# Optimization experiments

Hardware: AMD Instinct MI355X
Metric: run time of the kernel (lower is better)

Reference implementation:

```python
import jax, jax.numpy as jnp
import numpy as np

T, B, E, H, V = 256, 256, 256, 512, 50257
FORGET_BIAS = 1.0  # tf BasicLSTMCell default


def setup_inputs() -> dict:
    key = jax.random.key(0)
    k1, k2, k3, k4 = jax.random.split(key, 4)
    x = jax.random.normal(k1, (T, B, E), dtype=jnp.float32)
    # BasicLSTMCell kernel: [(E+H), 4H], gate order i, j, f, o
    lstm_kernel = jax.random.normal(k2, (E + H, 4 * H), dtype=jnp.float32) * 0.05
    lstm_bias = jnp.zeros((4 * H,), dtype=jnp.float32)
    W_out = jax.random.normal(k3, (H, V), dtype=jnp.float32) * 0.05
    b_out = jax.random.normal(k4, (V,), dtype=jnp.float32) * 0.05
    return {"x": x, "lstm_kernel": lstm_kernel, "lstm_bias": lstm_bias,
            "W_out": W_out, "b_out": b_out}


def reference(x, lstm_kernel, lstm_bias, W_out, b_out):
    # x: [T, B, E] (static_rnn list of timesteps). BasicLSTMCell recurrence.
    h0 = jnp.zeros((x.shape[1], H), dtype=x.dtype)
    c0 = jnp.zeros_like(h0)

    def step(carry, x_t):
        h, c = carry
        gates = jnp.concatenate([x_t, h], axis=-1) @ lstm_kernel + lstm_bias
        i, j, f, o = jnp.split(gates, 4, axis=-1)  # tf gate order: i, j, f, o
        c_new = jax.nn.sigmoid(f + FORGET_BIAS) * c + jax.nn.sigmoid(i) * jnp.tanh(j)
        h_new = jax.nn.sigmoid(o) * jnp.tanh(c_new)
        return (h_new, c_new), None

    (h_last, _), _ = jax.lax.scan(step, (h0, c0), x)
    # Final dense projection on last output only
    return h_last @ W_out + b_out  # [B, V]
```

## Files before the change

### kernel.cpp

```cpp
#include <hip/hip_runtime.h>
#include <hip/hip_bf16.h>

#define T_DIM 256
#define B_DIM 256
#define E_DIM 256
#define H_DIM 512
#define V_DIM 50257
#define BH    (B_DIM * H_DIM)
#define PRE_AHEAD 5
#define SENT  0x7F7F7F7Fu

typedef __attribute__((ext_vector_type(8))) short short8;
typedef __attribute__((ext_vector_type(4))) float f32x4;
typedef __attribute__((ext_vector_type(4))) unsigned int uint4v;
typedef __attribute__((ext_vector_type(2))) unsigned int uint2v;

__device__ __forceinline__ unsigned short f2bf(float f) {
    union { float f; unsigned u; } v; v.f = f;
    unsigned r = v.u + 0x7FFFu + ((v.u >> 16) & 1u);
    return (unsigned short)(r >> 16);
}
__device__ __forceinline__ short cvt_bf(float f) { return (short)f2bf(f); }
__device__ __forceinline__ float sigmoidf_(float x) {
    return 1.0f / (1.0f + __expf(-x));
}
__device__ __forceinline__ float tanhf_(float x) {
    float xc = fminf(fmaxf(x, -15.0f), 15.0f);
    float e = __expf(2.0f * xc);
    return (e - 1.0f) / (e + 1.0f);
}

__device__ __forceinline__ short8 load16_mall(const unsigned short* p) {
    short8 r;
    asm volatile("global_load_dwordx4 %0, %1, off sc0 sc1"
                 : "=v"(r) : "v"(p) : "memory");
    return r;
}
__device__ __forceinline__ void store8_mall(unsigned short* p, uint2v v) {
    asm volatile("global_store_dwordx2 %0, %1, off sc0 sc1"
                 :: "v"(p), "v"(v) : "memory");
}
__device__ __forceinline__ bool frag_ready(short8 v) {
    union { short8 s; uint4v u; } c; c.s = v;
    return (c.u[0] != SENT) & (c.u[1] != SENT) & (c.u[2] != SENT) & (c.u[3] != SENT);
}

__global__ void __launch_bounds__(128, 1)
lstm_persist(const float* __restrict__ x,
             const float* __restrict__ wk,
             const float* __restrict__ bias,
             unsigned short* __restrict__ hbuf)
{
    extern __shared__ unsigned short lds_w[];
    const int tid = threadIdx.x;
    const int blk = blockIdx.x;
    const int bg  = blk & 7;
    const int hg  = blk >> 3;
    const int bb  = bg * 32;
    const int hh  = hg * 16;

    for (int f = 0; f < 96; ++f) {
        const int kt = f >> 2, g = f & 3;
        for (int idx = tid; idx < 512; idx += 128) {
            const int c  = idx & 15;
            const int hi = (idx >> 4) & 3;
            const int j  = idx >> 6;
            const int k  = kt * 32 + hi * 8 + j;
            const int col = g * 512 + hh + c;
            lds_w[(f * 64 + hi * 16 + c) * 8 + j] = f2bf(wk[(size_t)k * 2048 + col]);
        }
    }
    __syncthreads();

    const int w    = tid >> 6;
    const int lane = tid & 63;
    const int lc   = lane & 15;
    const int lk   = lane >> 4;

    const f32x4 bi  = *(const f32x4*)(bias + 0 * 512 + hh + lk * 4);
    const f32x4 bj  = *(const f32x4*)(bias + 1 * 512 + hh + lk * 4);
    f32x4       bf_ = *(const f32x4*)(bias + 2 * 512 + hh + lk * 4);
    const f32x4 bo  = *(const f32x4*)(bias + 3 * 512 + hh + lk * 4);
    bf_ = bf_ + 1.0f;

    f32x4 c_frag = {0.f, 0.f, 0.f, 0.f};

    const int arow = bb + w * 16 + lc;
    const float* xbase = x + (size_t)arow * E_DIM + lk * 8;
    const size_t hrow_off = (size_t)arow * H_DIM + lk * 8;
    const size_t hsto_off = (size_t)arow * H_DIM + hh + lk * 4;

    f32x4 xreg[16];
    #pragma unroll
    for (int kt = 0; kt < 8; ++kt) {
        const float* p = xbase + kt * 32;
        xreg[2 * kt]     = *(const f32x4*)p;
        xreg[2 * kt + 1] = *(const f32x4*)(p + 4);
    }

    const uint2v sentv = {SENT, SENT};

    for (int t = 0; t < T_DIM; ++t) {
        f32x4 a0 = {0.f,0.f,0.f,0.f}, a1 = a0, a2 = a0, a3 = a0;
        short8 apk[8];
        #pragma unroll
        for (int kt = 0; kt < 8; ++kt) {
            const f32x4 lo = xreg[2 * kt];
            const f32x4 hi = xreg[2 * kt + 1];
            short8 a;
            a[0]=cvt_bf(lo[0]); a[1]=cvt_bf(lo[1]); a[2]=cvt_bf(lo[2]); a[3]=cvt_bf(lo[3]);
            a[4]=cvt_bf(hi[0]); a[5]=cvt_bf(hi[1]); a[6]=cvt_bf(hi[2]); a[7]=cvt_bf(hi[3]);
            apk[kt] = a;
        }
        #pragma unroll
        for (int kt = 0; kt < 8; ++kt) {
            const unsigned short* wp = lds_w + ((size_t)(kt * 4) * 64 + lane) * 8;
            a0 = __builtin_amdgcn_mfma_f32_16x16x32_bf16(*(const short8*)(wp +    0), apk[kt], a0, 0,0,0);
            a1 = __builtin_amdgcn_mfma_f32_16x16x32_bf16(*(const short8*)(wp +  512), apk[kt], a1, 0,0,0);
            a2 = __builtin_amdgcn_mfma_f32_16x16x32_bf16(*(const short8*)(wp + 1024), apk[kt], a2, 0,0,0);
            a3 = __builtin_amdgcn_mfma_f32_16x16x32_bf16(*(const short8*)(wp + 1536), apk[kt], a3, 0,0,0);
        }

        if (t + 1 < T_DIM) {
            const float* xn = xbase + (size_t)(t + 1) * (B_DIM * E_DIM);
            #pragma unroll
            for (int kt = 0; kt < 8; ++kt) {
                const float* p = xn + kt * 32;
                xreg[2 * kt]     = *(const f32x4*)p;
                xreg[2 * kt + 1] = *(const f32x4*)(p + 4);
            }
        }

        if (t > 0) {
            const unsigned short* hr = hbuf + (size_t)t * BH + hrow_off;
            short8 hfr[16];
            #pragma unroll
            for (int k = 0; k < 16; ++k)
                hfr[k] = load16_mall(hr + k * 32);
            asm volatile("s_waitcnt vmcnt(0)" ::: "memory");
            __builtin_amdgcn_sched_barrier(0);

            unsigned pend = 0;
            #pragma unroll
            for (int k = 0; k < 16; ++k)
                pend |= frag_ready(hfr[k]) ? 0u : (1u << k);
            #pragma unroll 1
            while (!__all(pend == 0)) {
                #pragma unroll
                for (int k = 0; k < 16; ++k)
                    if (pend & (1u << k)) hfr[k] = load16_mall(hr + k * 32);
                asm volatile("s_waitcnt vmcnt(0)" ::: "memory");
                __builtin_amdgcn_sched_barrier(0);
                unsigned np = 0;
                #pragma unroll
                for (int k = 0; k < 16; ++k)
                    if (pend & (1u << k))
                        np |= frag_ready(hfr[k]) ? 0u : (1u << k);
                pend = np;
            }
            __builtin_amdgcn_sched_barrier(0);

            #pragma unroll
            for (int k = 0; k < 16; ++k) {
                const unsigned short* wp = lds_w + ((size_t)((8 + k) * 4) * 64 + lane) * 8;
                a0 = __builtin_amdgcn_mfma_f32_16x16x32_bf16(*(const short8*)(wp +    0), hfr[k], a0, 0,0,0);
                a1 = __builtin_amdgcn_mfma_f32_16x16x32_bf16(*(const short8*)(wp +  512), hfr[k], a1, 0,0,0);
                a2 = __builtin_amdgcn_mfma_f32_16x16x32_bf16(*(const short8*)(wp + 1024), hfr[k], a2, 0,0,0);
                a3 = __builtin_amdgcn_mfma_f32_16x16x32_bf16(*(const short8*)(wp + 1536), hfr[k], a3, 0,0,0);
            }
        }

        unsigned short hu[4];
        #pragma unroll
        for (int j = 0; j < 4; ++j) {
            const float iv = a0[j] + bi[j];
            const float jv = a1[j] + bj[j];
            const float fv = a2[j] + bf_[j];
            const float ov = a3[j] + bo[j];
            const float cn = sigmoidf_(fv) * c_frag[j] + sigmoidf_(iv) * tanhf_(jv);
            c_frag[j] = cn;
            hu[j] = f2bf(sigmoidf_(ov) * tanhf_(cn));
        }
        uint2v pk;
        pk[0] = (unsigned)hu[0] | ((unsigned)hu[1] << 16);
        pk[1] = (unsigned)hu[2] | ((unsigned)hu[3] << 16);
        store8_mall(hbuf + (size_t)(t + 1) * BH + hsto_off, pk);
        if (t + PRE_AHEAD <= T_DIM)
            store8_mall(hbuf + (size_t)(t + PRE_AHEAD) * BH + hsto_off, sentv);
    }
}

__global__ void __launch_bounds__(256)
proj_gemm(const unsigned short* __restrict__ h,
          const float* __restrict__ wout,
          const float* __restrict__ bout,
          float* __restrict__ out)
{
    const int tid  = threadIdx.x;
    const int w    = tid >> 6;
    const int lane = tid & 63;
    const int lc   = lane & 15;
    const int lk   = lane >> 4;
    const int n0   = blockIdx.x * 128 + w * 32;

    f32x4 acc[16][2];
    #pragma unroll
    for (int mt = 0; mt < 16; ++mt) {
        acc[mt][0] = (f32x4){0.f,0.f,0.f,0.f};
        acc[mt][1] = (f32x4){0.f,0.f,0.f,0.f};
    }
    int ncl[2];
    ncl[0] = min(n0 + lc,      V_DIM - 1);
    ncl[1] = min(n0 + 16 + lc, V_DIM - 1);

    #pragma unroll 4
    for (int kt = 0; kt < 16; ++kt) {
        short8 bfr[2];
        #pragma unroll
        for (int nt = 0; nt < 2; ++nt) {
            #pragma unroll
            for (int j = 0; j < 8; ++j) {
                const int k = kt * 32 + lk * 8 + j;
                bfr[nt][j] = (short)f2bf(wout[(size_t)k * V_DIM + ncl[nt]]);
            }
        }
        #pragma unroll
        for (int mt = 0; mt < 16; ++mt) {
            const short8 a = *(const short8*)(h + (size_t)(mt * 16 + lc) * H_DIM
                                                + kt * 32 + lk * 8);
            acc[mt][0] = __builtin_amdgcn_mfma_f32_16x16x32_bf16(a, bfr[0], acc[mt][0], 0,0,0);
            acc[mt][1] = __builtin_amdgcn_mfma_f32_16x16x32_bf16(a, bfr[1], acc[mt][1], 0,0,0);
        }
    }

    #pragma unroll
    for (int nt = 0; nt < 2; ++nt) {
        const int n = n0 + nt * 16 + lc;
        if (n < V_DIM) {
            const float bb = bout[n];
            #pragma unroll
            for (int mt = 0; mt < 16; ++mt)
                #pragma unroll
                for (int j = 0; j < 4; ++j)
                    out[(size_t)(mt * 16 + lk * 4 + j) * V_DIM + n] = acc[mt][nt][j] + bb;
        }
    }
}

extern "C" void kernel_launch(void* const* d_in, const int* in_sizes, int n_in,
                              void* d_out, int out_size, void* d_ws, size_t ws_size,
                              hipStream_t stream) {
    const float* x    = (const float*)d_in[0];
    const float* wk   = (const float*)d_in[1];
    const float* bias = (const float*)d_in[2];
    const float* wout = (const float*)d_in[3];
    const float* bout = (const float*)d_in[4];
    float* out = (float*)d_out;

    unsigned short* hbuf = (unsigned short*)d_ws;

    hipMemsetAsync(hbuf, 0x7F, (size_t)PRE_AHEAD * BH * 2, stream);

    hipFuncSetAttribute((const void*)lstm_persist,
                        hipFuncAttributeMaxDynamicSharedMemorySize, 96 * 1024);

    hipLaunchKernelGGL(lstm_persist, dim3(256), dim3(128), 96 * 1024, stream,
                       x, wk, bias, hbuf);
    hipLaunchKernelGGL(proj_gemm, dim3((V_DIM + 127) / 128), dim3(256), 0, stream,
                       hbuf + (size_t)T_DIM * BH, wout, bout, out);
}
```

Measured before the change: 1.557 ms.

## Issue h loads early and overlap with x-part MFMAs via double-buffered x registers

Restructures the persistent LSTM step so the next-timestep x prefetch and the h-state fragment loads are issued before the x-contribution MFMAs. The spin-wait on sentinels then runs only after those MFMAs, hiding global/MALL latency behind compute. The x prefetch registers are double-buffered (xA/xB, loop unrolled by two) so the prefetch no longer overwrites the registers in use. This raises register pressure, and the x-part MFMAs now sit in the dependency window of the h loads.

```diff
diff --git a/kernel.cpp b/kernel.cpp
--- a/kernel.cpp
+++ b/kernel.cpp
@@ -15,6 +15,8 @@
 typedef __attribute__((ext_vector_type(4))) unsigned int uint4v;
 typedef __attribute__((ext_vector_type(2))) unsigned int uint2v;
 
+#define MFMA __builtin_amdgcn_mfma_f32_16x16x32_bf16
+
 __device__ __forceinline__ unsigned short f2bf(float f) {
     union { float f; unsigned u; } v; v.f = f;
     unsigned r = v.u + 0x7FFFu + ((v.u >> 16) & 1u);
@@ -43,6 +45,105 @@
 __device__ __forceinline__ bool frag_ready(short8 v) {
     union { short8 s; uint4v u; } c; c.s = v;
     return (c.u[0] != SENT) & (c.u[1] != SENT) & (c.u[2] != SENT) & (c.u[3] != SENT);
+}
+
+__device__ __forceinline__ void lstm_step(
+    int t, f32x4 (&xc)[16], f32x4 (&xn)[16],
+    const float* __restrict__ xrow,
+    unsigned short* __restrict__ hbuf,
+    size_t hrow_off, size_t hsto_off,
+    const unsigned short* __restrict__ lds_w, int lane,
+    const f32x4& bi, const f32x4& bj, const f32x4& bf_, const f32x4& bo,
+    f32x4& c_frag)
+{
+    {
+        const int tn = (t + 1 < T_DIM) ? t + 1 : t;
+        const float* xp = xrow + (size_t)tn * (B_DIM * E_DIM);
+        #pragma unroll
+        for (int k = 0; k < 8; ++k) {
+            xn[2 * k]     = *(const f32x4*)(xp + k * 32);
+            xn[2 * k + 1] = *(const f32x4*)(xp + k * 32 + 4);
+        }
+    }
+
+    const unsigned short* hr = hbuf + (size_t)t * BH + hrow_off;
+    short8 hfr[16];
+    if (t > 0) {
+        #pragma unroll
+        for (int k = 0; k < 16; ++k)
+            hfr[k] = load16_mall(hr + k * 32);
+    }
+
+    f32x4 a0 = {0.f,0.f,0.f,0.f}, a1 = a0, a2 = a0, a3 = a0;
+    #pragma unroll
+    for (int kt = 0; kt < 8; ++kt) {
+        const f32x4 lo = xc[2 * kt];
+        const f32x4 hi = xc[2 * kt + 1];
+        short8 a;
+        a[0]=cvt_bf(lo[0]); a[1]=cvt_bf(lo[1]); a[2]=cvt_bf(lo[2]); a[3]=cvt_bf(lo[3]);
+        a[4]=cvt_bf(hi[0]); a[5]=cvt_bf(hi[1]); a[6]=cvt_bf(hi[2]); a[7]=cvt_bf(hi[3]);
+        const unsigned short* wp = lds_w + ((size_t)(kt * 4) * 64 + lane) * 8;
+        a0 = MFMA(*(const short8*)(wp +    0), a, a0, 0,0,0);
+        a1 = MFMA(*(const short8*)(wp +  512), a, a1, 0,0,0);
+        a2 = MFMA(*(const short8*)(wp + 1024), a, a2, 0,0,0);
+        a3 = MFMA(*(const short8*)(wp + 1536), a, a3, 0,0,0);
+    }
+
+    if (t > 0) {
+        asm volatile("s_waitcnt vmcnt(0)" ::: "memory");
+        __builtin_amdgcn_sched_barrier(0);
+        unsigned pend = 0;
+        #pragma unroll
+        for (int k = 0; k < 16; ++k)
+            pend |= frag_ready(hfr[k]) ? 0u : (1u << k);
+        #pragma unroll 1
+        while (!__all(pend == 0)) {
+            #pragma unroll
+            for (int k = 0; k < 16; ++k)
+                if (pend & (1u << k)) hfr[k] = load16_mall(hr + k * 32);
+            asm volatile("s_waitcnt vmcnt(0)" ::: "memory");
+            __builtin_amdgcn_sched_barrier(0);
+            unsigned np = 0;
+            #pragma unroll
+            for (int k = 0; k < 16; ++k)
+                if (pend & (1u << k))
+                    np |= frag_ready(hfr[k]) ? 0u : (1u << k);
+            pend = np;
+        }
+        __builtin_amdgcn_sched_barrier(0);
+
+        #pragma unroll
+        for (int k = 0; k < 16; ++k) {
+            const unsigned short* wp = lds_w + ((size_t)((8 + k) * 4) * 64 + lane) * 8;
+            a0 = MFMA(*(const short8*)(wp +    0), hfr[k], a0, 0,0,0);
+            a1 = MFMA(*(const short8*)(wp +  512), hfr[k], a1, 0,0,0);
+            a2 = MFMA(*(const short8*)(wp + 1024), hfr[k], a2, 0,0,0);
+            a3 = MFMA(*(const short8*)(wp + 1536), hfr[k], a3, 0,0,0);
+        }
+    } else {
+        asm volatile("s_waitcnt vmcnt(0)" ::: "memory");
+        __builtin_amdgcn_sched_barrier(0);
+    }
+
+    unsigned short hu[4];
+    #pragma unroll
+    for (int j = 0; j < 4; ++j) {
+        const float iv = a0[j] + bi[j];
+        const float jv = a1[j] + bj[j];
+        const float fv = a2[j] + bf_[j];
+        const float ov = a3[j] + bo[j];
+        const float cn = sigmoidf_(fv) * c_frag[j] + sigmoidf_(iv) * tanhf_(jv);
+        c_frag[j] = cn;
+        hu[j] = f2bf(sigmoidf_(ov) * tanhf_(cn));
+    }
+    uint2v pk;
+    pk[0] = (unsigned)hu[0] | ((unsigned)hu[1] << 16);
+    pk[1] = (unsigned)hu[2] | ((unsigned)hu[3] << 16);
+    store8_mall(hbuf + (size_t)(t + 1) * BH + hsto_off, pk);
+    if (t + PRE_AHEAD <= T_DIM) {
+        const uint2v sentv = {SENT, SENT};
+        store8_mall(hbuf + (size_t)(t + PRE_AHEAD) * BH + hsto_off, sentv);
+    }
 }
 
 __global__ void __launch_bounds__(128, 1)
@@ -86,107 +187,22 @@
     f32x4 c_frag = {0.f, 0.f, 0.f, 0.f};
 
     const int arow = bb + w * 16 + lc;
-    const float* xbase = x + (size_t)arow * E_DIM + lk * 8;
+    const float* xrow = x + (size_t)arow * E_DIM + lk * 8;
     const size_t hrow_off = (size_t)arow * H_DIM + lk * 8;
     const size_t hsto_off = (size_t)arow * H_DIM + hh + lk * 4;
 
-    f32x4 xreg[16];
-    #pragma unroll
-    for (int kt = 0; kt < 8; ++kt) {
-        const float* p = xbase + kt * 32;
-        xreg[2 * kt]     = *(const f32x4*)p;
-        xreg[2 * kt + 1] = *(const f32x4*)(p + 4);
-    }
-
-    const uint2v sentv = {SENT, SENT};
-
-    for (int t = 0; t < T_DIM; ++t) {
-        f32x4 a0 = {0.f,0.f,0.f,0.f}, a1 = a0, a2 = a0, a3 = a0;
-        short8 apk[8];
-        #pragma unroll
-        for (int kt = 0; kt < 8; ++kt) {
-            const f32x4 lo = xreg[2 * kt];
-            const f32x4 hi = xreg[2 * kt + 1];
-            short8 a;
-            a[0]=cvt_bf(lo[0]); a[1]=cvt_bf(lo[1]); a[2]=cvt_bf(lo[2]); a[3]=cvt_bf(lo[3]);
-            a[4]=cvt_bf(hi[0]); a[5]=cvt_bf(hi[1]); a[6]=cvt_bf(hi[2]); a[7]=cvt_bf(hi[3]);
-            apk[kt] = a;
-        }
-        #pragma unroll
-        for (int kt = 0; kt < 8; ++kt) {
-            const unsigned short* wp = lds_w + ((size_t)(kt * 4) * 64 + lane) * 8;
-            a0 = __builtin_amdgcn_mfma_f32_16x16x32_bf16(*(const short8*)(wp +    0), apk[kt], a0, 0,0,0);
-            a1 = __builtin_amdgcn_mfma_f32_16x16x32_bf16(*(const short8*)(wp +  512), apk[kt], a1, 0,0,0);
-            a2 = __builtin_amdgcn_mfma_f32_16x16x32_bf16(*(const short8*)(wp + 1024), apk[kt], a2, 0,0,0);
-            a3 = __builtin_amdgcn_mfma_f32_16x16x32_bf16(*(const short8*)(wp + 1536), apk[kt], a3, 0,0,0);
-        }
-
-        if (t + 1 < T_DIM) {
-            const float* xn = xbase + (size_t)(t + 1) * (B_DIM * E_DIM);
-            #pragma unroll
-            for (int kt = 0; kt < 8; ++kt) {
-                const float* p = xn + kt * 32;
-                xreg[2 * kt]     = *(const f32x4*)p;
-                xreg[2 * kt + 1] = *(const f32x4*)(p + 4);
-            }
-        }
-
-        if (t > 0) {
-            const unsigned short* hr = hbuf + (size_t)t * BH + hrow_off;
-            short8 hfr[16];
-            #pragma unroll
-            for (int k = 0; k < 16; ++k)
-                hfr[k] = load16_mall(hr + k * 32);
-            asm volatile("s_waitcnt vmcnt(0)" ::: "memory");
-            __builtin_amdgcn_sched_barrier(0);
-
-            unsigned pend = 0;
-            #pragma unroll
-            for (int k = 0; k < 16; ++k)
-                pend |= frag_ready(hfr[k]) ? 0u : (1u << k);
-            #pragma unroll 1
-            while (!__all(pend == 0)) {
-                #pragma unroll
-                for (int k = 0; k < 16; ++k)
-                    if (pend & (1u << k)) hfr[k] = load16_mall(hr + k * 32);
-                asm volatile("s_waitcnt vmcnt(0)" ::: "memory");
-                __builtin_amdgcn_sched_barrier(0);
-                unsigned np = 0;
-                #pragma unroll
-                for (int k = 0; k < 16; ++k)
-                    if (pend & (1u << k))
-                        np |= frag_ready(hfr[k]) ? 0u : (1u << k);
-                pend = np;
-            }
-            __builtin_amdgcn_sched_barrier(0);
-
-            #pragma unroll
-            for (int k = 0; k < 16; ++k) {
-                const unsigned short* wp = lds_w + ((size_t)((8 + k) * 4) * 64 + lane) * 8;
-                a0 = __builtin_amdgcn_mfma_f32_16x16x32_bf16(*(const short8*)(wp +    0), hfr[k], a0, 0,0,0);
-                a1 = __builtin_amdgcn_mfma_f32_16x16x32_bf16(*(const short8*)(wp +  512), hfr[k], a1, 0,0,0);
-                a2 = __builtin_amdgcn_mfma_f32_16x16x32_bf16(*(const short8*)(wp + 1024), hfr[k], a2, 0,0,0);
-                a3 = __builtin_amdgcn_mfma_f32_16x16x32_bf16(*(const short8*)(wp + 1536), hfr[k], a3, 0,0,0);
-            }
-        }
-
-        unsigned short hu[4];
-        #pragma unroll
-        for (int j = 0; j < 4; ++j) {
-            const float iv = a0[j] + bi[j];
-            const float jv = a1[j] + bj[j];
-            const float fv = a2[j] + bf_[j];
-            const float ov = a3[j] + bo[j];
-            const float cn = sigmoidf_(fv) * c_frag[j] + sigmoidf_(iv) * tanhf_(jv);
-            c_frag[j] = cn;
-            hu[j] = f2bf(sigmoidf_(ov) * tanhf_(cn));
-        }
-        uint2v pk;
-        pk[0] = (unsigned)hu[0] | ((unsigned)hu[1] << 16);
-        pk[1] = (unsigned)hu[2] | ((unsigned)hu[3] << 16);
-        store8_mall(hbuf + (size_t)(t + 1) * BH + hsto_off, pk);
-        if (t + PRE_AHEAD <= T_DIM)
-            store8_mall(hbuf + (size_t)(t + PRE_AHEAD) * BH + hsto_off, sentv);
+    f32x4 xA[16], xB[16];
+    #pragma unroll
+    for (int k = 0; k < 8; ++k) {
+        xA[2 * k]     = *(const f32x4*)(xrow + k * 32);
+        xA[2 * k + 1] = *(const f32x4*)(xrow + k * 32 + 4);
+    }
+
+    for (int tb = 0; tb < T_DIM; tb += 2) {
+        lstm_step(tb,     xA, xB, xrow, hbuf, hrow_off, hsto_off,
+                  lds_w, lane, bi, bj, bf_, bo, c_frag);
+        lstm_step(tb + 1, xB, xA, xrow, hbuf, hrow_off, hsto_off,
+                  lds_w, lane, bi, bj, bf_, bo, c_frag);
     }
 }
 
@@ -228,8 +244,8 @@
         for (int mt = 0; mt < 16; ++mt) {
             const short8 a = *(const short8*)(h + (size_t)(mt * 16 + lc) * H_DIM
                                                 + kt * 32 + lk * 8);
-            acc[mt][0] = __builtin_amdgcn_mfma_f32_16x16x32_bf16(a, bfr[0], acc[mt][0], 0,0,0);
-            acc[mt][1] = __builtin_amdgcn_mfma_f32_16x16x32_bf16(a, bfr[1], acc[mt][1], 0,0,0);
+            acc[mt][0] = MFMA(a, bfr[0], acc[mt][0], 0,0,0);
+            acc[mt][1] = MFMA(a, bfr[1], acc[mt][1], 0,0,0);
         }
     }
 
```

Result: slower. 1.954 ms (+25.5%).

## Route same-XCC hidden-state exchange through local L2 ring buffer

Applied to the files above, without the earlier changes.

Each persistent block records its XCC id in a table. Consumers then work out which h fragments come from producers on the same XCC and read those from an 8-slot ring buffer with L2-scoped loads and stores, while cross-XCC fragments still go through the MALL-coherent buffer. The goal is lower latency for the per-step recurrent dependency. In exchange it adds a second store per step, extra sentinel arming, two more memsets, and a startup handshake. Correctness now depends on L2 coherence within an XCC and on the ring depth being enough to avoid overwriting slots that are still in use.

```diff
diff --git a/kernel.cpp b/kernel.cpp
--- a/kernel.cpp
+++ b/kernel.cpp
@@ -7,6 +7,8 @@
 #define H_DIM 512
 #define V_DIM 50257
 #define BH    (B_DIM * H_DIM)
+#define RINGL 8
+#define ARM_L 3
 #define PRE_AHEAD 5
 #define SENT  0x7F7F7F7Fu
 
@@ -14,6 +16,8 @@
 typedef __attribute__((ext_vector_type(4))) float f32x4;
 typedef __attribute__((ext_vector_type(4))) unsigned int uint4v;
 typedef __attribute__((ext_vector_type(2))) unsigned int uint2v;
+
+#define MFMA __builtin_amdgcn_mfma_f32_16x16x32_bf16
 
 __device__ __forceinline__ unsigned short f2bf(float f) {
     union { float f; unsigned u; } v; v.f = f;
@@ -36,8 +40,29 @@
                  : "=v"(r) : "v"(p) : "memory");
     return r;
 }
+__device__ __forceinline__ short8 load16_loc(const unsigned short* p) {
+    short8 r;
+    asm volatile("global_load_dwordx4 %0, %1, off sc0"
+                 : "=v"(r) : "v"(p) : "memory");
+    return r;
+}
 __device__ __forceinline__ void store8_mall(unsigned short* p, uint2v v) {
     asm volatile("global_store_dwordx2 %0, %1, off sc0 sc1"
+                 :: "v"(p), "v"(v) : "memory");
+}
+__device__ __forceinline__ void store8_loc(unsigned short* p, uint2v v) {
+    asm volatile("global_store_dwordx2 %0, %1, off"
+                 :: "v"(p), "v"(v) : "memory");
+}
+__device__ __forceinline__ int load_int_mall(const int* p) {
+    int r;
+    asm volatile("global_load_dword %0, %1, off sc0 sc1\n\t"
+                 "s_waitcnt vmcnt(0)"
+                 : "=v"(r) : "v"(p) : "memory");
+    return r;
+}
+__device__ __forceinline__ void store_int_mall(int* p, int v) {
+    asm volatile("global_store_dword %0, %1, off sc0 sc1"
                  :: "v"(p), "v"(v) : "memory");
 }
 __device__ __forceinline__ bool frag_ready(short8 v) {
@@ -49,7 +74,9 @@
 lstm_persist(const float* __restrict__ x,
              const float* __restrict__ wk,
              const float* __restrict__ bias,
-             unsigned short* __restrict__ hbuf)
+             unsigned short* __restrict__ hbuf_m,
+             unsigned short* __restrict__ hbuf_l,
+             int* __restrict__ xcctab)
 {
     extern __shared__ unsigned short lds_w[];
     const int tid = threadIdx.x;
@@ -58,6 +85,11 @@
     const int hg  = blk >> 3;
     const int bb  = bg * 32;
     const int hh  = hg * 16;
+
+    unsigned xcc;
+    asm volatile("s_getreg_b32 %0, hwreg(HW_REG_XCC_ID)" : "=s"(xcc));
+    if (tid == 0)
+        store_int_mall(xcctab + bg * 512 + hg * 16, (int)(xcc & 7u));
 
     for (int f = 0; f < 96; ++f) {
         const int kt = f >> 2, g = f & 3;
@@ -77,6 +109,24 @@
     const int lc   = lane & 15;
     const int lk   = lane >> 4;
 
+    unsigned fragmask = 0;
+    {
+        const int* tp = xcctab + bg * 512 + (lane & 31) * 16;
+        int e = -1;
+        #pragma unroll 1
+        for (int it = 0; it < 256; ++it) {
+            e = load_int_mall(tp);
+            if (__all(e != -1)) break;
+            __builtin_amdgcn_s_sleep(8);
+        }
+        if (__all(e != -1)) {
+            const int p0 = __shfl(e, 2 * (lane & 15));
+            const int p1 = __shfl(e, 2 * (lane & 15) + 1);
+            const bool loc = (p0 == (int)(xcc & 7u)) && (p1 == (int)(xcc & 7u));
+            fragmask = (unsigned)(__ballot(loc) & 0xFFFFull);
+        }
+    }
+
     const f32x4 bi  = *(const f32x4*)(bias + 0 * 512 + hh + lk * 4);
     const f32x4 bj  = *(const f32x4*)(bias + 1 * 512 + hh + lk * 4);
     f32x4       bf_ = *(const f32x4*)(bias + 2 * 512 + hh + lk * 4);
@@ -86,16 +136,15 @@
     f32x4 c_frag = {0.f, 0.f, 0.f, 0.f};
 
     const int arow = bb + w * 16 + lc;
-    const float* xbase = x + (size_t)arow * E_DIM + lk * 8;
+    const float* xrow = x + (size_t)arow * E_DIM + lk * 8;
     const size_t hrow_off = (size_t)arow * H_DIM + lk * 8;
     const size_t hsto_off = (size_t)arow * H_DIM + hh + lk * 4;
 
     f32x4 xreg[16];
     #pragma unroll
-    for (int kt = 0; kt < 8; ++kt) {
-        const float* p = xbase + kt * 32;
-        xreg[2 * kt]     = *(const f32x4*)p;
-        xreg[2 * kt + 1] = *(const f32x4*)(p + 4);
+    for (int k = 0; k < 8; ++k) {
+        xreg[2 * k]     = *(const f32x4*)(xrow + k * 32);
+        xreg[2 * k + 1] = *(const f32x4*)(xrow + k * 32 + 4);
     }
 
     const uint2v sentv = {SENT, SENT};
@@ -115,28 +164,30 @@
         #pragma unroll
         for (int kt = 0; kt < 8; ++kt) {
             const unsigned short* wp = lds_w + ((size_t)(kt * 4) * 64 + lane) * 8;
-            a0 = __builtin_amdgcn_mfma_f32_16x16x32_bf16(*(const short8*)(wp +    0), apk[kt], a0, 0,0,0);
-            a1 = __builtin_amdgcn_mfma_f32_16x16x32_bf16(*(const short8*)(wp +  512), apk[kt], a1, 0,0,0);
-            a2 = __builtin_amdgcn_mfma_f32_16x16x32_bf16(*(const short8*)(wp + 1024), apk[kt], a2, 0,0,0);
-            a3 = __builtin_amdgcn_mfma_f32_16x16x32_bf16(*(const short8*)(wp + 1536), apk[kt], a3, 0,0,0);
+            a0 = MFMA(*(const short8*)(wp +    0), apk[kt], a0, 0,0,0);
+            a1 = MFMA(*(const short8*)(wp +  512), apk[kt], a1, 0,0,0);
+            a2 = MFMA(*(const short8*)(wp + 1024), apk[kt], a2, 0,0,0);
+            a3 = MFMA(*(const short8*)(wp + 1536), apk[kt], a3, 0,0,0);
         }
 
         if (t + 1 < T_DIM) {
-            const float* xn = xbase + (size_t)(t + 1) * (B_DIM * E_DIM);
-            #pragma unroll
-            for (int kt = 0; kt < 8; ++kt) {
-                const float* p = xn + kt * 32;
-                xreg[2 * kt]     = *(const f32x4*)p;
-                xreg[2 * kt + 1] = *(const f32x4*)(p + 4);
+            const float* xn = xrow + (size_t)(t + 1) * (B_DIM * E_DIM);
+            #pragma unroll
+            for (int k = 0; k < 8; ++k) {
+                xreg[2 * k]     = *(const f32x4*)(xn + k * 32);
+                xreg[2 * k + 1] = *(const f32x4*)(xn + k * 32 + 4);
             }
         }
 
         if (t > 0) {
-            const unsigned short* hr = hbuf + (size_t)t * BH + hrow_off;
+            const unsigned short* hr_l = hbuf_l + (size_t)(t & (RINGL - 1)) * BH + hrow_off;
+            const unsigned short* hr_m = hbuf_m + (size_t)t * BH + hrow_off;
             short8 hfr[16];
             #pragma unroll
-            for (int k = 0; k < 16; ++k)
-                hfr[k] = load16_mall(hr + k * 32);
+            for (int k = 0; k < 16; ++k) {
+                if ((fragmask >> k) & 1) hfr[k] = load16_loc(hr_l + k * 32);
+                else                     hfr[k] = load16_mall(hr_m + k * 32);
+            }
             asm volatile("s_waitcnt vmcnt(0)" ::: "memory");
             __builtin_amdgcn_sched_barrier(0);
 
@@ -144,11 +195,17 @@
             #pragma unroll
             for (int k = 0; k < 16; ++k)
                 pend |= frag_ready(hfr[k]) ? 0u : (1u << k);
+            int round = 0;
             #pragma unroll 1
             while (!__all(pend == 0)) {
                 #pragma unroll
                 for (int k = 0; k < 16; ++k)
-                    if (pend & (1u << k)) hfr[k] = load16_mall(hr + k * 32);
+                    if (pend & (1u << k)) {
+                        if (round == 0 && ((fragmask >> k) & 1))
+                            hfr[k] = load16_loc(hr_l + k * 32);
+                        else
+                            hfr[k] = load16_mall(hr_m + k * 32);
+                    }
                 asm volatile("s_waitcnt vmcnt(0)" ::: "memory");
                 __builtin_amdgcn_sched_barrier(0);
                 unsigned np = 0;
@@ -157,16 +214,17 @@
                     if (pend & (1u << k))
                         np |= frag_ready(hfr[k]) ? 0u : (1u << k);
                 pend = np;
+                ++round;
             }
             __builtin_amdgcn_sched_barrier(0);
 
             #pragma unroll
             for (int k = 0; k < 16; ++k) {
                 const unsigned short* wp = lds_w + ((size_t)((8 + k) * 4) * 64 + lane) * 8;
-                a0 = __builtin_amdgcn_mfma_f32_16x16x32_bf16(*(const short8*)(wp +    0), hfr[k], a0, 0,0,0);
-                a1 = __builtin_amdgcn_mfma_f32_16x16x32_bf16(*(const short8*)(wp +  512), hfr[k], a1, 0,0,0);
-                a2 = __builtin_amdgcn_mfma_f32_16x16x32_bf16(*(const short8*)(wp + 1024), hfr[k], a2, 0,0,0);
-                a3 = __builtin_amdgcn_mfma_f32_16x16x32_bf16(*(const short8*)(wp + 1536), hfr[k], a3, 0,0,0);
+                a0 = MFMA(*(const short8*)(wp +    0), hfr[k], a0, 0,0,0);
+                a1 = MFMA(*(const short8*)(wp +  512), hfr[k], a1, 0,0,0);
+                a2 = MFMA(*(const short8*)(wp + 1024), hfr[k], a2, 0,0,0);
+                a3 = MFMA(*(const short8*)(wp + 1536), hfr[k], a3, 0,0,0);
             }
         }
 
@@ -184,9 +242,12 @@
         uint2v pk;
         pk[0] = (unsigned)hu[0] | ((unsigned)hu[1] << 16);
         pk[1] = (unsigned)hu[2] | ((unsigned)hu[3] << 16);
-        store8_mall(hbuf + (size_t)(t + 1) * BH + hsto_off, pk);
+        store8_loc (hbuf_l + (size_t)((t + 1) & (RINGL - 1)) * BH + hsto_off, pk);
+        store8_mall(hbuf_m + (size_t)(t + 1) * BH + hsto_off, pk);
+        if (t + ARM_L < T_DIM)
+            store8_loc(hbuf_l + (size_t)((t + ARM_L) & (RINGL - 1)) * BH + hsto_off, sentv);
         if (t + PRE_AHEAD <= T_DIM)
-            store8_mall(hbuf + (size_t)(t + PRE_AHEAD) * BH + hsto_off, sentv);
+            store8_mall(hbuf_m + (size_t)(t + PRE_AHEAD) * BH + hsto_off, sentv);
     }
 }
 
@@ -228,8 +289,8 @@
         for (int mt = 0; mt < 16; ++mt) {
             const short8 a = *(const short8*)(h + (size_t)(mt * 16 + lc) * H_DIM
                                                 + kt * 32 + lk * 8);
-            acc[mt][0] = __builtin_amdgcn_mfma_f32_16x16x32_bf16(a, bfr[0], acc[mt][0], 0,0,0);
-            acc[mt][1] = __builtin_amdgcn_mfma_f32_16x16x32_bf16(a, bfr[1], acc[mt][1], 0,0,0);
+            acc[mt][0] = MFMA(a, bfr[0], acc[mt][0], 0,0,0);
+            acc[mt][1] = MFMA(a, bfr[1], acc[mt][1], 0,0,0);
         }
     }
 
@@ -257,15 +318,19 @@
     const float* bout = (const float*)d_in[4];
     float* out = (float*)d_out;
 
-    unsigned short* hbuf = (unsigned short*)d_ws;
-
-    hipMemsetAsync(hbuf, 0x7F, (size_t)PRE_AHEAD * BH * 2, stream);
+    unsigned short* hbuf_m = (unsigned short*)d_ws;
+    unsigned short* hbuf_l = (unsigned short*)((char*)d_ws + (size_t)(T_DIM + 1) * BH * 2);
+    int*            xcctab = (int*)((char*)hbuf_l + (size_t)RINGL * BH * 2);
+
+    hipMemsetAsync(hbuf_m, 0x7F, (size_t)PRE_AHEAD * BH * 2, stream);
+    hipMemsetAsync(hbuf_l, 0x7F, (size_t)RINGL * BH * 2, stream);
+    hipMemsetAsync(xcctab, 0xFF, 8 * 32 * 16 * sizeof(int), stream);
 
     hipFuncSetAttribute((const void*)lstm_persist,
                         hipFuncAttributeMaxDynamicSharedMemorySize, 96 * 1024);
 
     hipLaunchKernelGGL(lstm_persist, dim3(256), dim3(128), 96 * 1024, stream,
-                       x, wk, bias, hbuf);
+                       x, wk, bias, hbuf_m, hbuf_l, xcctab);
     hipLaunchKernelGGL(proj_gemm, dim3((V_DIM + 127) / 128), dim3(256), 0, stream,
-                       hbuf + (size_t)T_DIM * BH, wout, bout, out);
-}
+                       hbuf_m + (size_t)T_DIM * BH, wout, bout, out);
+}
```

New measurement: 1.768 ms. +13.5%, slower.

## Split LSTM hidden columns over 512 blocks with ring buffer and gate shuffles

Applied to the files above, without the earlier changes.

Doubles the persistent LSTM grid to 512 blocks, each owning 8 hidden columns instead of 16. Each wave now issues half as many MFMAs per step, and gate values are exchanged across wave halves with a lane shuffle. The hidden-state history becomes a 16-slot ring buffer instead of a full T-length buffer. The change also adds s_setprio around the MFMA loops and swaps x conversion to the library bf16 conversion. The gain relies on all 512 blocks being co-resident for the spin-wait sync, so more blocks poll the sentinel flags each step. The sentinel-prefill memset still covers only 5 slots, and it is unclear whether the ring reuse and the projection reading slot 0 are correct.

```diff
diff --git a/kernel.cpp b/kernel.cpp
--- a/kernel.cpp
+++ b/kernel.cpp
@@ -7,6 +7,7 @@
 #define H_DIM 512
 #define V_DIM 50257
 #define BH    (B_DIM * H_DIM)
+#define RING  16
 #define PRE_AHEAD 5
 #define SENT  0x7F7F7F7Fu
 
@@ -15,12 +16,17 @@
 typedef __attribute__((ext_vector_type(4))) unsigned int uint4v;
 typedef __attribute__((ext_vector_type(2))) unsigned int uint2v;
 
+#define MFMA __builtin_amdgcn_mfma_f32_16x16x32_bf16
+
 __device__ __forceinline__ unsigned short f2bf(float f) {
     union { float f; unsigned u; } v; v.f = f;
     unsigned r = v.u + 0x7FFFu + ((v.u >> 16) & 1u);
     return (unsigned short)(r >> 16);
 }
-__device__ __forceinline__ short cvt_bf(float f) { return (short)f2bf(f); }
+__device__ __forceinline__ short cvt_bf(float f) {
+    __hip_bfloat16 h = __float2bfloat16(f);
+    return *reinterpret_cast<short*>(&h);
+}
 __device__ __forceinline__ float sigmoidf_(float x) {
     return 1.0f / (1.0f + __expf(-x));
 }
@@ -54,20 +60,21 @@
     extern __shared__ unsigned short lds_w[];
     const int tid = threadIdx.x;
     const int blk = blockIdx.x;
-    const int bg  = blk & 7;
-    const int hg  = blk >> 3;
+    const int b8  = blk >> 8;
+    const int bg  = (blk & 7) ^ b8;
+    const int hg  = ((blk >> 3) & 31) | (b8 << 5);
     const int bb  = bg * 32;
-    const int hh  = hg * 16;
-
-    for (int f = 0; f < 96; ++f) {
-        const int kt = f >> 2, g = f & 3;
+    const int hh  = hg * 8;
+
+    for (int f = 0; f < 48; ++f) {
+        const int kt = f >> 1, n = f & 1;
         for (int idx = tid; idx < 512; idx += 128) {
-            const int c  = idx & 15;
-            const int hi = (idx >> 4) & 3;
-            const int j  = idx >> 6;
-            const int k  = kt * 32 + hi * 8 + j;
-            const int col = g * 512 + hh + c;
-            lds_w[(f * 64 + hi * 16 + c) * 8 + j] = f2bf(wk[(size_t)k * 2048 + col]);
+            const int l   = idx & 63;
+            const int j   = idx >> 6;
+            const int c16 = l & 15;
+            const int k   = kt * 32 + (l >> 4) * 8 + j;
+            const int col = (n * 2 + (c16 >> 3)) * 512 + hh + (c16 & 7);
+            lds_w[(f * 64 + l) * 8 + j] = f2bf(wk[(size_t)k * 2048 + col]);
         }
     }
     __syncthreads();
@@ -76,32 +83,33 @@
     const int lane = tid & 63;
     const int lc   = lane & 15;
     const int lk   = lane >> 4;
-
-    const f32x4 bi  = *(const f32x4*)(bias + 0 * 512 + hh + lk * 4);
-    const f32x4 bj  = *(const f32x4*)(bias + 1 * 512 + hh + lk * 4);
-    f32x4       bf_ = *(const f32x4*)(bias + 2 * 512 + hh + lk * 4);
-    const f32x4 bo  = *(const f32x4*)(bias + 3 * 512 + hh + lk * 4);
+    const int hb4  = (lk & 1) * 4;
+    const bool glo = (lane & 32) == 0;
+
+    const f32x4 bi  = *(const f32x4*)(bias + 0 * 512 + hh + hb4);
+    const f32x4 bj  = *(const f32x4*)(bias + 1 * 512 + hh + hb4);
+    f32x4       bf_ = *(const f32x4*)(bias + 2 * 512 + hh + hb4);
+    const f32x4 bo  = *(const f32x4*)(bias + 3 * 512 + hh + hb4);
     bf_ = bf_ + 1.0f;
 
     f32x4 c_frag = {0.f, 0.f, 0.f, 0.f};
 
     const int arow = bb + w * 16 + lc;
-    const float* xbase = x + (size_t)arow * E_DIM + lk * 8;
+    const float* xrow = x + (size_t)arow * E_DIM + lk * 8;
     const size_t hrow_off = (size_t)arow * H_DIM + lk * 8;
-    const size_t hsto_off = (size_t)arow * H_DIM + hh + lk * 4;
+    const size_t hsto_off = (size_t)arow * H_DIM + hh + hb4;
 
     f32x4 xreg[16];
     #pragma unroll
-    for (int kt = 0; kt < 8; ++kt) {
-        const float* p = xbase + kt * 32;
-        xreg[2 * kt]     = *(const f32x4*)p;
-        xreg[2 * kt + 1] = *(const f32x4*)(p + 4);
+    for (int k = 0; k < 8; ++k) {
+        xreg[2 * k]     = *(const f32x4*)(xrow + k * 32);
+        xreg[2 * k + 1] = *(const f32x4*)(xrow + k * 32 + 4);
     }
 
     const uint2v sentv = {SENT, SENT};
 
     for (int t = 0; t < T_DIM; ++t) {
-        f32x4 a0 = {0.f,0.f,0.f,0.f}, a1 = a0, a2 = a0, a3 = a0;
+        f32x4 a0 = {0.f,0.f,0.f,0.f}, a1 = a0;
         short8 apk[8];
         #pragma unroll
         for (int kt = 0; kt < 8; ++kt) {
@@ -112,27 +120,26 @@
             a[4]=cvt_bf(hi[0]); a[5]=cvt_bf(hi[1]); a[6]=cvt_bf(hi[2]); a[7]=cvt_bf(hi[3]);
             apk[kt] = a;
         }
+        __builtin_amdgcn_s_setprio(1);
         #pragma unroll
         for (int kt = 0; kt < 8; ++kt) {
-            const unsigned short* wp = lds_w + ((size_t)(kt * 4) * 64 + lane) * 8;
-            a0 = __builtin_amdgcn_mfma_f32_16x16x32_bf16(*(const short8*)(wp +    0), apk[kt], a0, 0,0,0);
-            a1 = __builtin_amdgcn_mfma_f32_16x16x32_bf16(*(const short8*)(wp +  512), apk[kt], a1, 0,0,0);
-            a2 = __builtin_amdgcn_mfma_f32_16x16x32_bf16(*(const short8*)(wp + 1024), apk[kt], a2, 0,0,0);
-            a3 = __builtin_amdgcn_mfma_f32_16x16x32_bf16(*(const short8*)(wp + 1536), apk[kt], a3, 0,0,0);
-        }
+            const unsigned short* wp = lds_w + ((size_t)(kt * 2) * 64 + lane) * 8;
+            a0 = MFMA(*(const short8*)(wp +   0), apk[kt], a0, 0,0,0);
+            a1 = MFMA(*(const short8*)(wp + 512), apk[kt], a1, 0,0,0);
+        }
+        __builtin_amdgcn_s_setprio(0);
 
         if (t + 1 < T_DIM) {
-            const float* xn = xbase + (size_t)(t + 1) * (B_DIM * E_DIM);
-            #pragma unroll
-            for (int kt = 0; kt < 8; ++kt) {
-                const float* p = xn + kt * 32;
-                xreg[2 * kt]     = *(const f32x4*)p;
-                xreg[2 * kt + 1] = *(const f32x4*)(p + 4);
+            const float* xn = xrow + (size_t)(t + 1) * (B_DIM * E_DIM);
+            #pragma unroll
+            for (int k = 0; k < 8; ++k) {
+                xreg[2 * k]     = *(const f32x4*)(xn + k * 32);
+                xreg[2 * k + 1] = *(const f32x4*)(xn + k * 32 + 4);
             }
         }
 
         if (t > 0) {
-            const unsigned short* hr = hbuf + (size_t)t * BH + hrow_off;
+            const unsigned short* hr = hbuf + (size_t)(t & (RING - 1)) * BH + hrow_off;
             short8 hfr[16];
             #pragma unroll
             for (int k = 0; k < 16; ++k)
@@ -160,33 +167,42 @@
             }
             __builtin_amdgcn_sched_barrier(0);
 
+            __builtin_amdgcn_s_setprio(1);
             #pragma unroll
             for (int k = 0; k < 16; ++k) {
-                const unsigned short* wp = lds_w + ((size_t)((8 + k) * 4) * 64 + lane) * 8;
-                a0 = __builtin_amdgcn_mfma_f32_16x16x32_bf16(*(const short8*)(wp +    0), hfr[k], a0, 0,0,0);
-                a1 = __builtin_amdgcn_mfma_f32_16x16x32_bf16(*(const short8*)(wp +  512), hfr[k], a1, 0,0,0);
-                a2 = __builtin_amdgcn_mfma_f32_16x16x32_bf16(*(const short8*)(wp + 1024), hfr[k], a2, 0,0,0);
-                a3 = __builtin_amdgcn_mfma_f32_16x16x32_bf16(*(const short8*)(wp + 1536), hfr[k], a3, 0,0,0);
-            }
-        }
-
+                const unsigned short* wp = lds_w + ((size_t)((8 + k) * 2) * 64 + lane) * 8;
+                a0 = MFMA(*(const short8*)(wp +   0), hfr[k], a0, 0,0,0);
+                a1 = MFMA(*(const short8*)(wp + 512), hfr[k], a1, 0,0,0);
+            }
+            __builtin_amdgcn_s_setprio(0);
+        }
+
+        f32x4 p0, p1;
+        #pragma unroll
+        for (int j = 0; j < 4; ++j) {
+            p0[j] = __shfl_xor(a0[j], 32);
+            p1[j] = __shfl_xor(a1[j], 32);
+        }
         unsigned short hu[4];
         #pragma unroll
         for (int j = 0; j < 4; ++j) {
-            const float iv = a0[j] + bi[j];
-            const float jv = a1[j] + bj[j];
-            const float fv = a2[j] + bf_[j];
-            const float ov = a3[j] + bo[j];
+            const float iv = (glo ? a0[j] : p0[j]) + bi[j];
+            const float jv = (glo ? p0[j] : a0[j]) + bj[j];
+            const float fv = (glo ? a1[j] : p1[j]) + bf_[j];
+            const float ov = (glo ? p1[j] : a1[j]) + bo[j];
             const float cn = sigmoidf_(fv) * c_frag[j] + sigmoidf_(iv) * tanhf_(jv);
             c_frag[j] = cn;
-            hu[j] = f2bf(sigmoidf_(ov) * tanhf_(cn));
-        }
-        uint2v pk;
-        pk[0] = (unsigned)hu[0] | ((unsigned)hu[1] << 16);
-        pk[1] = (unsigned)hu[2] | ((unsigned)hu[3] << 16);
-        store8_mall(hbuf + (size_t)(t + 1) * BH + hsto_off, pk);
-        if (t + PRE_AHEAD <= T_DIM)
-            store8_mall(hbuf + (size_t)(t + PRE_AHEAD) * BH + hsto_off, sentv);
+            hu[j] = (unsigned short)cvt_bf(sigmoidf_(ov) * tanhf_(cn));
+        }
+
+        if (glo) {
+            uint2v pk;
+            pk[0] = (unsigned)hu[0] | ((unsigned)hu[1] << 16);
+            pk[1] = (unsigned)hu[2] | ((unsigned)hu[3] << 16);
+            store8_mall(hbuf + (size_t)((t + 1) & (RING - 1)) * BH + hsto_off, pk);
+            if (t + PRE_AHEAD <= T_DIM)
+                store8_mall(hbuf + (size_t)((t + PRE_AHEAD) & (RING - 1)) * BH + hsto_off, sentv);
+        }
     }
 }
 
@@ -228,8 +244,8 @@
         for (int mt = 0; mt < 16; ++mt) {
             const short8 a = *(const short8*)(h + (size_t)(mt * 16 + lc) * H_DIM
                                                 + kt * 32 + lk * 8);
-            acc[mt][0] = __builtin_amdgcn_mfma_f32_16x16x32_bf16(a, bfr[0], acc[mt][0], 0,0,0);
-            acc[mt][1] = __builtin_amdgcn_mfma_f32_16x16x32_bf16(a, bfr[1], acc[mt][1], 0,0,0);
+            acc[mt][0] = MFMA(a, bfr[0], acc[mt][0], 0,0,0);
+            acc[mt][1] = MFMA(a, bfr[1], acc[mt][1], 0,0,0);
         }
     }
 
@@ -262,10 +278,10 @@
     hipMemsetAsync(hbuf, 0x7F, (size_t)PRE_AHEAD * BH * 2, stream);
 
     hipFuncSetAttribute((const void*)lstm_persist,
-                        hipFuncAttributeMaxDynamicSharedMemorySize, 96 * 1024);
-
-    hipLaunchKernelGGL(lstm_persist, dim3(256), dim3(128), 96 * 1024, stream,
+                        hipFuncAttributeMaxDynamicSharedMemorySize, 48 * 1024);
+
+    hipLaunchKernelGGL(lstm_persist, dim3(512), dim3(128), 48 * 1024, stream,
                        x, wk, bias, hbuf);
     hipLaunchKernelGGL(proj_gemm, dim3((V_DIM + 127) / 128), dim3(256), 0, stream,
-                       hbuf + (size_t)T_DIM * BH, wout, bout, out);
-}
+                       hbuf, wout, bout, out);
+}
```

After: 2.312 ms. +48.5%, slower.
